# Optimization experiments

Hardware: AMD Instinct MI355X
Metric: run time of the kernel (lower is better)

Reference implementation:

```python
import jax, jax.numpy as jnp
import numpy as np

B, H, W, C = 32, 56, 56, 384
NH, WS, SS = 12, 7, 3
DH = C // NH
N = WS * WS
HID = 4 * C
SCALE = DH ** -0.5


def _make_attn_mask(h, w, ws, ss):
    img = np.zeros((h, w), dtype=np.float32)
    cnt = 0
    for hs in (slice(0, -ws), slice(-ws, -ss), slice(-ss, None)):
        for wsl in (slice(0, -ws), slice(-ws, -ss), slice(-ss, None)):
            img[hs, wsl] = cnt
            cnt += 1
    mw = img.reshape(h // ws, ws, w // ws, ws).transpose(0, 2, 1, 3).reshape(-1, ws * ws)
    diff = mw[:, None, :] - mw[:, :, None]  # (nW, n, n)
    return np.where(diff != 0, np.float32(-100.0), np.float32(0.0))


def _make_rel_pos_index(ws):
    coords = np.stack(np.meshgrid(np.arange(ws), np.arange(ws), indexing='ij')).reshape(2, -1)
    rel = (coords[:, :, None] - coords[:, None, :]).transpose(1, 2, 0)  # (n, n, 2)
    rel[..., 0] += ws - 1
    rel[..., 1] += ws - 1
    rel[..., 0] *= 2 * ws - 1
    return rel.sum(-1)  # (n, n)


ATTN_MASK = jnp.asarray(_make_attn_mask(H, W, WS, SS))          # (nW, n, n)
REL_IDX = jnp.asarray(_make_rel_pos_index(WS))                   # (n, n)


def layernorm(x, g, b, eps):
    mu = jnp.mean(x, axis=-1, keepdims=True)
    var = jnp.var(x, axis=-1, keepdims=True)
    return (x - mu) * jax.lax.rsqrt(var + eps) * g + b


def window_partition(x, ws):
    b, h, w, c = x.shape
    x = x.reshape(b, h // ws, ws, w // ws, ws, c)
    return x.transpose(0, 1, 3, 2, 4, 5).reshape(-1, ws, ws, c)


def window_reverse(windows, ws, h, w):
    b = windows.shape[0] // ((h // ws) * (w // ws))
    x = windows.reshape(b, h // ws, w // ws, ws, ws, -1)
    return x.transpose(0, 1, 3, 2, 4, 5).reshape(b, h, w, -1)


def setup_inputs() -> dict:
    key = jax.random.key(0)
    ks = jax.random.split(key, 8)
    d = {
        'x': jax.random.normal(ks[0], (B, H * W, C), dtype=jnp.float32),
        'ln1_g': jnp.ones((C,), jnp.float32), 'ln1_b': jnp.zeros((C,), jnp.float32),
        'qkv_w': jax.random.normal(ks[1], (C, 3 * C), jnp.float32) * 0.02,
        'qkv_b': jnp.zeros((3 * C,), jnp.float32),
        'proj_w': jax.random.normal(ks[2], (C, C), jnp.float32) * 0.02,
        'proj_b': jnp.zeros((C,), jnp.float32),
        'rpb_table': jax.random.normal(ks[3], ((2 * WS - 1) ** 2, NH), jnp.float32) * 0.02,
        'ln2_g': jnp.ones((C,), jnp.float32), 'ln2_b': jnp.zeros((C,), jnp.float32),
        'ffln_g': jnp.ones((C,), jnp.float32), 'ffln_b': jnp.zeros((C,), jnp.float32),
        'ff1_w': jax.random.normal(ks[4], (C, HID), jnp.float32) * 0.02,
        'ff1_b': jnp.zeros((HID,), jnp.float32),
        'ff2_w': jax.random.normal(ks[5], (HID, C), jnp.float32) * 0.02,
        'ff2_b': jnp.zeros((C,), jnp.float32),
    }
    return d


def reference(x, ln1_g, ln1_b, qkv_w, qkv_b, proj_w, proj_b, rpb_table,
              ln2_g, ln2_b, ffln_g, ffln_b, ff1_w, ff1_b, ff2_w, ff2_b):
    b = x.shape[0]
    shortcut = x
    xn = layernorm(x, ln1_g, ln1_b, 1e-5).reshape(b, H, W, C)
    shifted = jnp.roll(xn, shift=(-SS, -SS), axis=(1, 2))
    xw = window_partition(shifted, WS).reshape(-1, N, C)  # (b*nW, n, c)
    Bw = xw.shape[0]
    nW = Bw // b

    qkv = (xw @ qkv_w + qkv_b).reshape(Bw, N, 3, NH, DH).transpose(2, 0, 3, 1, 4)
    q, k, v = qkv[0], qkv[1], qkv[2]  # (Bw, nh, n, dh)
    dots = jnp.einsum('bhnd,bhmd->bhnm', q, k) * SCALE

    bias = rpb_table[REL_IDX.reshape(-1)].reshape(N, N, NH).transpose(2, 0, 1)  # (nh, n, n)
    attn = dots + bias[None]
    attn = attn.reshape(b, nW, NH, N, N) + ATTN_MASK[None, :, None, :, :]
    attn = jax.nn.softmax(attn.reshape(Bw, NH, N, N), axis=-1)

    out = jnp.einsum('bhnm,bhmd->bhnd', attn, v)
    out = out.transpose(0, 2, 1, 3).reshape(Bw, N, C)
    out = out @ proj_w + proj_b

    out = window_reverse(out.reshape(-1, WS, WS, C), WS, H, W)
    out = jnp.roll(out, shift=(SS, SS), axis=(1, 2)).reshape(b, H * W, C)

    x = shortcut + out
    y = layernorm(x, ln2_g, ln2_b, 1e-5)
    y = layernorm(y, ffln_g, ffln_b, 1e-6)
    y = jax.nn.gelu(y @ ff1_w + ff1_b, approximate=False) @ ff2_w + ff2_b
    return x + y
```

## Files before the change

### kernel.cpp

```cpp
#include <hip/hip_runtime.h>
#include <hip/hip_bf16.h>

typedef short bf16x8 __attribute__((ext_vector_type(8)));
typedef float f32x4  __attribute__((ext_vector_type(4)));

static constexpr float SCALE = 0.17677669529663687f;

__device__ __forceinline__ void gload_lds16(const void* g, void* l) {
  __builtin_amdgcn_global_load_lds(
      (const __attribute__((address_space(1))) unsigned int*)g,
      (__attribute__((address_space(3))) unsigned int*)l, 16, 0, 0);
}

__device__ __forceinline__ size_t win_to_nat(int t) {
  int win = t / 49; int n = t - win * 49;
  int bb = win >> 6; int wimg = win & 63;
  int hb = wimg >> 3, wb = wimg & 7;
  int nr = n / 7, nc = n - nr * 7;
  int hh = hb * 7 + nr + 3; if (hh >= 56) hh -= 56;
  int ww = wb * 7 + nc + 3; if (ww >= 56) ww -= 56;
  return (size_t)bb * 3136 + (size_t)hh * 56 + ww;
}

__global__ __launch_bounds__(256)
void k_transpose(const float* __restrict__ W, __hip_bfloat16* __restrict__ Wt,
                 int K, int N) {
  __shared__ float tile[32][33];
  int tx = threadIdx.x & 31, ty = threadIdx.x >> 5;
  int tc = blockIdx.x, tr = blockIdx.y;
#pragma unroll
  for (int r = 0; r < 32; r += 8)
    tile[r + ty][tx] = W[(size_t)(tr * 32 + r + ty) * N + tc * 32 + tx];
  __syncthreads();
#pragma unroll
  for (int r = 0; r < 32; r += 8)
    Wt[(size_t)(tc * 32 + r + ty) * K + tr * 32 + tx] =
        __float2bfloat16(tile[tx][r + ty]);
}

__global__ __launch_bounds__(256)
void k_ln1(const float* __restrict__ x, const float* __restrict__ gw,
           const float* __restrict__ bw, __hip_bfloat16* __restrict__ xw) {
  int lane = threadIdx.x & 63;
  int t = blockIdx.x * 4 + (threadIdx.x >> 6);
  size_t nt = win_to_nat(t);
  const float* xr = x + nt * 384;
  float4 a  = *(const float4*)(xr + lane * 4);
  float2 c2 = *(const float2*)(xr + 256 + lane * 2);
  float v[6] = {a.x, a.y, a.z, a.w, c2.x, c2.y};
  int c0 = lane * 4, c1 = 256 + lane * 2;
  int ch[6] = {c0, c0 + 1, c0 + 2, c0 + 3, c1, c1 + 1};
  float s = 0.f, q = 0.f;
#pragma unroll
  for (int i = 0; i < 6; i++) { s += v[i]; q += v[i] * v[i]; }
#pragma unroll
  for (int m = 1; m < 64; m <<= 1) { s += __shfl_xor(s, m); q += __shfl_xor(q, m); }
  float mean = s * (1.f / 384.f);
  float rstd = rsqrtf(q * (1.f / 384.f) - mean * mean + 1e-5f);
  __hip_bfloat16* o = xw + (size_t)t * 384;
#pragma unroll
  for (int i = 0; i < 6; i++)
    o[ch[i]] = __float2bfloat16((v[i] - mean) * rstd * gw[ch[i]] + bw[ch[i]]);
}

__global__ __launch_bounds__(256)
void k_ln2ff(const float* __restrict__ xres, const float* __restrict__ g2,
             const float* __restrict__ b2, const float* __restrict__ gf,
             const float* __restrict__ bf_, __hip_bfloat16* __restrict__ yln) {
  int lane = threadIdx.x & 63;
  int t = blockIdx.x * 4 + (threadIdx.x >> 6);
  const float* xr = xres + (size_t)t * 384;
  float4 a  = *(const float4*)(xr + lane * 4);
  float2 c2 = *(const float2*)(xr + 256 + lane * 2);
  float v[6] = {a.x, a.y, a.z, a.w, c2.x, c2.y};
  int c0 = lane * 4, c1 = 256 + lane * 2;
  int ch[6] = {c0, c0 + 1, c0 + 2, c0 + 3, c1, c1 + 1};
  float s = 0.f, q = 0.f;
#pragma unroll
  for (int i = 0; i < 6; i++) { s += v[i]; q += v[i] * v[i]; }
#pragma unroll
  for (int m = 1; m < 64; m <<= 1) { s += __shfl_xor(s, m); q += __shfl_xor(q, m); }
  float mean = s * (1.f / 384.f);
  float rstd = rsqrtf(q * (1.f / 384.f) - mean * mean + 1e-5f);
  float y1[6];
  s = 0.f; q = 0.f;
#pragma unroll
  for (int i = 0; i < 6; i++) {
    y1[i] = (v[i] - mean) * rstd * g2[ch[i]] + b2[ch[i]];
    s += y1[i]; q += y1[i] * y1[i];
  }
#pragma unroll
  for (int m = 1; m < 64; m <<= 1) { s += __shfl_xor(s, m); q += __shfl_xor(q, m); }
  float m2 = s * (1.f / 384.f);
  float r2 = rsqrtf(q * (1.f / 384.f) - m2 * m2 + 1e-6f);
  __hip_bfloat16* o = yln + (size_t)t * 384;
#pragma unroll
  for (int i = 0; i < 6; i++)
    o[ch[i]] = __float2bfloat16((y1[i] - m2) * r2 * gf[ch[i]] + bf_[ch[i]]);
}

enum { EPI_QKV = 0, EPI_PROJ = 1, EPI_FF1 = 2, EPI_FF2 = 3 };

template <int EPI>
__global__ __launch_bounds__(256)
void k_gemm(const __hip_bfloat16* __restrict__ A, const __hip_bfloat16* __restrict__ Wt,
            const float* __restrict__ bias, int K, int nCol, int cpx,
            const float* __restrict__ aux,
            float* __restrict__ out_f,
            __hip_bfloat16* __restrict__ out_b) {
  __shared__ __hip_bfloat16 As[2][8192];
  __shared__ __hip_bfloat16 Bs[2][8192];
  int tid = threadIdx.x;
  int lane = tid & 63, w = tid >> 6;
  int g = lane >> 4, r16 = lane & 15;
  int wr = w >> 1, wc = w & 1;

  int bid = blockIdx.x;
  int wg = (bid & 7) * cpx + (bid >> 3);
  int rB = wg / nCol;
  int rowBlk = rB * 128;
  int colBlk = (wg - rB * nCol) * 128;

  int srow = tid >> 3;
  int cch = (tid & 7) ^ (srow & 7);
  const __hip_bfloat16* PA = A + (size_t)(rowBlk + srow) * K + cch * 8;
  const __hip_bfloat16* PB = Wt + (size_t)(colBlk + srow) * K + cch * 8;

#define STG(NB, T)                                                      \
  {                                                                     \
    int k0s = (T) << 6;                                                 \
    _Pragma("unroll") for (int j = 0; j < 4; j++) {                     \
      gload_lds16(PA + (size_t)j * 32 * K + k0s, &As[NB][j * 2048 + w * 512]); \
      gload_lds16(PB + (size_t)j * 32 * K + k0s, &Bs[NB][j * 2048 + w * 512]); \
    }                                                                   \
  }

  int aBase = (wr * 64 + r16) * 64;
  int bBase = (wc * 64 + r16) * 64;
  int sw0 = (g ^ (r16 & 7)) * 8;
  int sw1 = ((4 + g) ^ (r16 & 7)) * 8;

  f32x4 acc[4][4] = {};
  const int nt = K >> 6;

  STG(0, 0)

  for (int t = 0; t < nt; ++t) {
    int cur = t & 1;
    if (t + 1 < nt) {
      STG(cur ^ 1, t + 1)
      asm volatile("s_waitcnt vmcnt(8)" ::: "memory");
    } else {
      asm volatile("s_waitcnt vmcnt(0)" ::: "memory");
    }
    __builtin_amdgcn_s_barrier();

    bf16x8 a0[4], a1[4], b0[4], b1[4];
#pragma unroll
    for (int mi = 0; mi < 4; mi++) {
      a0[mi] = *(const bf16x8*)(&As[cur][aBase + mi * 1024 + sw0]);
      a1[mi] = *(const bf16x8*)(&As[cur][aBase + mi * 1024 + sw1]);
    }
#pragma unroll
    for (int ni = 0; ni < 4; ni++) {
      b0[ni] = *(const bf16x8*)(&Bs[cur][bBase + ni * 1024 + sw0]);
      b1[ni] = *(const bf16x8*)(&Bs[cur][bBase + ni * 1024 + sw1]);
    }
    __builtin_amdgcn_s_setprio(1);
#pragma unroll
    for (int mi = 0; mi < 4; mi++)
#pragma unroll
      for (int ni = 0; ni < 4; ni++) {
        acc[mi][ni] = __builtin_amdgcn_mfma_f32_16x16x32_bf16(a0[mi], b0[ni], acc[mi][ni], 0, 0, 0);
        acc[mi][ni] = __builtin_amdgcn_mfma_f32_16x16x32_bf16(a1[mi], b1[ni], acc[mi][ni], 0, 0, 0);
      }
    __builtin_amdgcn_s_setprio(0);
    __builtin_amdgcn_s_barrier();
  }
#undef STG

#pragma unroll
  for (int mi = 0; mi < 4; mi++) {
#pragma unroll
    for (int rr = 0; rr < 4; rr++) {
      int row = rowBlk + wr * 64 + mi * 16 + g * 4 + rr;
      int winr = 0, nn = 0; size_t nt2 = 0;
      if constexpr (EPI == EPI_QKV) { winr = row / 49; nn = row - winr * 49; }
      if constexpr (EPI == EPI_PROJ) { nt2 = win_to_nat(row); }
#pragma unroll
      for (int ni = 0; ni < 4; ni++) {
        int col = colBlk + wc * 64 + ni * 16 + r16;
        float val = acc[mi][ni][rr] + bias[col];
        if constexpr (EPI == EPI_QKV) {
          int which = col / 384; int rem = col - which * 384;
          int hh = rem >> 5, dd = rem & 31;
          size_t off = (((size_t)winr * 12 + hh) * 49 + nn) * 32 + dd;
          out_b[(size_t)which * 38535168u + off] = __float2bfloat16(val);
        } else if constexpr (EPI == EPI_PROJ) {
          out_f[nt2 * 384 + col] = val + aux[nt2 * 384 + col];
        } else if constexpr (EPI == EPI_FF1) {
          float u = val * (val * val * 0.044715f + 1.0f) * 1.5957691216f;
          float e = __expf(u);
          float th = 1.f - 2.f / (e + 1.f);
          float ge = 0.5f * val * (1.f + th);
          out_b[(size_t)row * 1536 + col] = __float2bfloat16(ge);
        } else {
          out_f[(size_t)row * 384 + col] = val + aux[(size_t)row * 384 + col];
        }
      }
    }
  }
}

__global__ __launch_bounds__(256)
void k_attn(const __hip_bfloat16* __restrict__ q, const __hip_bfloat16* __restrict__ k,
            const __hip_bfloat16* __restrict__ v, const float* __restrict__ rpb,
            __hip_bfloat16* __restrict__ o) {
  __shared__ __hip_bfloat16 P[4][64][72];
  int tid = threadIdx.x;
  int lane = tid & 63, wave = tid >> 6;
  int g = lane >> 4, r16 = lane & 15;
  int gid = blockIdx.x * 4 + wave;
  int wi = gid / 12, h = gid - (gid / 12) * 12;
  int wimg = wi & 63;
  int hb = wimg >> 3, wb = wimg & 7;
  size_t base = ((size_t)wi * 12 + h) * (49 * 32);
  const __hip_bfloat16* qb = q + base;
  const __hip_bfloat16* kb = k + base;
  const __hip_bfloat16* vb = v + base;

  bf16x8 zf = {0, 0, 0, 0, 0, 0, 0, 0};
  bf16x8 qf[4], kf[4];
#pragma unroll
  for (int mi = 0; mi < 4; mi++) {
    int row = mi * 16 + r16;
    qf[mi] = (row < 49) ? *(const bf16x8*)(qb + row * 32 + g * 8) : zf;
    kf[mi] = (row < 49) ? *(const bf16x8*)(kb + row * 32 + g * 8) : zf;
  }
  f32x4 fz = {0.f, 0.f, 0.f, 0.f};
  f32x4 S[4][4];
#pragma unroll
  for (int mi = 0; mi < 4; mi++)
#pragma unroll
    for (int ni = 0; ni < 4; ni++)
      S[mi][ni] = __builtin_amdgcn_mfma_f32_16x16x32_bf16(qf[mi], kf[ni], fz, 0, 0, 0);

  int kiA[4], kjA[4], rkA[4], cvA[4];
#pragma unroll
  for (int ni = 0; ni < 4; ni++) {
    int col = ni * 16 + r16;
    cvA[ni] = (col < 49);
    int ki = col / 7, kj = col - (col / 7) * 7;
    kiA[ni] = ki; kjA[ni] = kj;
    int hg = hb * 7 + ki, wg = wb * 7 + kj;
    int rh = (hg < 49) ? 0 : ((hg < 53) ? 1 : 2);
    int rw = (wg < 49) ? 0 : ((wg < 53) ? 1 : 2);
    rkA[ni] = rh * 3 + rw;
  }

#pragma unroll
  for (int mi = 0; mi < 4; mi++) {
#pragma unroll
    for (int rr = 0; rr < 4; rr++) {
      int row = mi * 16 + g * 4 + rr;
      float sv[4];
      float mx = -1e30f;
      int qi = row / 7, qj = row - (row / 7) * 7;
      int hgq = hb * 7 + qi, wgq = wb * 7 + qj;
      int rhq = (hgq < 49) ? 0 : ((hgq < 53) ? 1 : 2);
      int rwq = (wgq < 49) ? 0 : ((wgq < 53) ? 1 : 2);
      int rq = rhq * 3 + rwq;
#pragma unroll
      for (int ni = 0; ni < 4; ni++) {
        float s = -1e30f;
        if (row < 49 && cvA[ni]) {
          int idx = (qi - kiA[ni] + 6) * 13 + (qj - kjA[ni] + 6);
          float maskv = (rq != rkA[ni]) ? -100.f : 0.f;
          s = S[mi][ni][rr] * SCALE + rpb[idx * 12 + h] + maskv;
        }
        sv[ni] = s;
        mx = fmaxf(mx, s);
      }
#pragma unroll
      for (int m = 1; m <= 8; m <<= 1) mx = fmaxf(mx, __shfl_xor(mx, m));
      float sum = 0.f;
#pragma unroll
      for (int ni = 0; ni < 4; ni++) {
        float p = __expf(sv[ni] - mx);
        sv[ni] = p; sum += p;
      }
#pragma unroll
      for (int m = 1; m <= 8; m <<= 1) sum += __shfl_xor(sum, m);
      float inv = 1.f / sum;
#pragma unroll
      for (int ni = 0; ni < 4; ni++)
        P[wave][row][ni * 16 + r16] = __float2bfloat16(sv[ni] * inv);
    }
  }

  f32x4 O[4][2] = {};
#pragma unroll
  for (int ks = 0; ks < 2; ks++) {
    bf16x8 pf[4];
#pragma unroll
    for (int mi = 0; mi < 4; mi++)
      pf[mi] = *(const bf16x8*)(&P[wave][mi * 16 + r16][ks * 32 + g * 8]);
#pragma unroll
    for (int ni = 0; ni < 2; ni++) {
      bf16x8 vf = zf;
#pragma unroll
      for (int j = 0; j < 8; j++) {
        int m = ks * 32 + g * 8 + j;
        if (m < 49) vf[j] = ((const short*)vb)[m * 32 + ni * 16 + r16];
      }
#pragma unroll
      for (int mi = 0; mi < 4; mi++)
        O[mi][ni] = __builtin_amdgcn_mfma_f32_16x16x32_bf16(pf[mi], vf, O[mi][ni], 0, 0, 0);
    }
  }

#pragma unroll
  for (int mi = 0; mi < 4; mi++)
#pragma unroll
    for (int rr = 0; rr < 4; rr++) {
      int row = mi * 16 + g * 4 + rr;
      if (row < 49) {
#pragma unroll
        for (int ni = 0; ni < 2; ni++) {
          int col = ni * 16 + r16;
          o[(((size_t)wi * 49 + row) * 12 + h) * 32 + col] = __float2bfloat16(O[mi][ni][rr]);
        }
      }
    }
}

extern "C" void kernel_launch(void* const* d_in, const int* in_sizes, int n_in,
                              void* d_out, int out_size, void* d_ws, size_t ws_size,
                              hipStream_t stream) {
  const float* x      = (const float*)d_in[0];
  const float* ln1_g  = (const float*)d_in[1];
  const float* ln1_b  = (const float*)d_in[2];
  const float* qkv_w  = (const float*)d_in[3];
  const float* qkv_b  = (const float*)d_in[4];
  const float* proj_w = (const float*)d_in[5];
  const float* proj_b = (const float*)d_in[6];
  const float* rpb    = (const float*)d_in[7];
  const float* ln2_g  = (const float*)d_in[8];
  const float* ln2_b  = (const float*)d_in[9];
  const float* ffg    = (const float*)d_in[10];
  const float* ffb    = (const float*)d_in[11];
  const float* ff1_w  = (const float*)d_in[12];
  const float* ff1_b  = (const float*)d_in[13];
  const float* ff2_w  = (const float*)d_in[14];
  const float* ff2_b  = (const float*)d_in[15];
  float* out = (float*)d_out;

  char* ws = (char*)d_ws;
  __hip_bfloat16* xw     = (__hip_bfloat16*)ws;
  __hip_bfloat16* qbuf   = (__hip_bfloat16*)(ws + 77070336u);
  __hip_bfloat16* kbuf   = qbuf + 38535168u;
  __hip_bfloat16* vbuf   = kbuf + 38535168u;
  __hip_bfloat16* attn_o = xw;
  __hip_bfloat16* hbuf   = (__hip_bfloat16*)ws;
  float*          x_res  = (float*)(ws + 308281344u);
  __hip_bfloat16* yln    = (__hip_bfloat16*)(ws + 462422016u);
  __hip_bfloat16* qkv_wt = (__hip_bfloat16*)(ws + 539492352u);
  __hip_bfloat16* proj_wt = qkv_wt + 442368u;
  __hip_bfloat16* ff1_wt  = proj_wt + 147456u;
  __hip_bfloat16* ff2_wt  = ff1_wt + 589824u;

  k_transpose<<<dim3(1152 / 32, 384 / 32), dim3(256), 0, stream>>>(qkv_w, qkv_wt, 384, 1152);
  k_transpose<<<dim3(384 / 32, 384 / 32), dim3(256), 0, stream>>>(proj_w, proj_wt, 384, 384);
  k_transpose<<<dim3(1536 / 32, 384 / 32), dim3(256), 0, stream>>>(ff1_w, ff1_wt, 384, 1536);
  k_transpose<<<dim3(384 / 32, 1536 / 32), dim3(256), 0, stream>>>(ff2_w, ff2_wt, 1536, 384);

  k_ln1<<<dim3(25088), dim3(256), 0, stream>>>(x, ln1_g, ln1_b, xw);

  k_gemm<EPI_QKV><<<dim3(7056), dim3(256), 0, stream>>>(xw, qkv_wt, qkv_b, 384, 9, 7056 / 8,
                                                        nullptr, nullptr, qbuf);
  k_attn<<<dim3(6144), dim3(256), 0, stream>>>(qbuf, kbuf, vbuf, rpb, attn_o);
  k_gemm<EPI_PROJ><<<dim3(2352), dim3(256), 0, stream>>>(attn_o, proj_wt, proj_b, 384, 3, 2352 / 8,
                                                         x, x_res, nullptr);
  k_ln2ff<<<dim3(25088), dim3(256), 0, stream>>>(x_res, ln2_g, ln2_b, ffg, ffb, yln);
  k_gemm<EPI_FF1><<<dim3(9408), dim3(256), 0, stream>>>(yln, ff1_wt, ff1_b, 384, 12, 9408 / 8,
                                                        nullptr, nullptr, hbuf);
  k_gemm<EPI_FF2><<<dim3(2352), dim3(256), 0, stream>>>(hbuf, ff2_wt, ff2_b, 1536, 3, 2352 / 8,
                                                        x_res, out, nullptr);
}
```

Measured before the change: 1.010 ms.

## Stage GEMM epilogue through LDS for vectorized coalesced global stores

The GEMM operand buffers are merged into one shared LDS array, and the MFMA operand order is swapped so each lane's accumulator holds four consecutive columns. After the main loop, each wave writes its biased (and, for FF1, GELU-applied) tile into its own swizzled LDS region. It then reads the tile back as 8-wide bf16 or 4-wide fp32 vectors for coalesced global stores and residual loads. This replaces scattered scalar stores in all four epilogues, at the cost of extra LDS traffic and register shuffling.

```diff
diff --git a/kernel.cpp b/kernel.cpp
--- a/kernel.cpp
+++ b/kernel.cpp
@@ -2,6 +2,7 @@
 #include <hip/hip_bf16.h>
 
 typedef short bf16x8 __attribute__((ext_vector_type(8)));
+typedef short short4v __attribute__((ext_vector_type(4)));
 typedef float f32x4  __attribute__((ext_vector_type(4)));
 
 static constexpr float SCALE = 0.17677669529663687f;
@@ -20,6 +21,13 @@
   int hh = hb * 7 + nr + 3; if (hh >= 56) hh -= 56;
   int ww = wb * 7 + nc + 3; if (ww >= 56) ww -= 56;
   return (size_t)bb * 3136 + (size_t)hh * 56 + ww;
+}
+
+__device__ __forceinline__ float gelu_tanh(float val) {
+  float u = val * (val * val * 0.044715f + 1.0f) * 1.5957691216f;
+  float e = __expf(u);
+  float th = 1.f - 2.f / (e + 1.f);
+  return 0.5f * val * (1.f + th);
 }
 
 __global__ __launch_bounds__(256)
@@ -108,8 +116,7 @@
             const float* __restrict__ aux,
             float* __restrict__ out_f,
             __hip_bfloat16* __restrict__ out_b) {
-  __shared__ __hip_bfloat16 As[2][8192];
-  __shared__ __hip_bfloat16 Bs[2][8192];
+  __shared__ __hip_bfloat16 LB[32768];
   int tid = threadIdx.x;
   int lane = tid & 63, w = tid >> 6;
   int g = lane >> 4, r16 = lane & 15;
@@ -126,13 +133,13 @@
   const __hip_bfloat16* PA = A + (size_t)(rowBlk + srow) * K + cch * 8;
   const __hip_bfloat16* PB = Wt + (size_t)(colBlk + srow) * K + cch * 8;
 
-#define STG(NB, T)                                                      \
-  {                                                                     \
-    int k0s = (T) << 6;                                                 \
-    _Pragma("unroll") for (int j = 0; j < 4; j++) {                     \
-      gload_lds16(PA + (size_t)j * 32 * K + k0s, &As[NB][j * 2048 + w * 512]); \
-      gload_lds16(PB + (size_t)j * 32 * K + k0s, &Bs[NB][j * 2048 + w * 512]); \
-    }                                                                   \
+#define STG(NB, T)                                                            \
+  {                                                                           \
+    int k0s = (T) << 6;                                                       \
+    _Pragma("unroll") for (int j = 0; j < 4; j++) {                           \
+      gload_lds16(PA + (size_t)j * 32 * K + k0s, &LB[(NB) * 8192 + j * 2048 + w * 512]); \
+      gload_lds16(PB + (size_t)j * 32 * K + k0s, &LB[16384 + (NB) * 8192 + j * 2048 + w * 512]); \
+    }                                                                         \
   }
 
   int aBase = (wr * 64 + r16) * 64;
@@ -158,55 +165,94 @@
     bf16x8 a0[4], a1[4], b0[4], b1[4];
 #pragma unroll
     for (int mi = 0; mi < 4; mi++) {
-      a0[mi] = *(const bf16x8*)(&As[cur][aBase + mi * 1024 + sw0]);
-      a1[mi] = *(const bf16x8*)(&As[cur][aBase + mi * 1024 + sw1]);
+      a0[mi] = *(const bf16x8*)(&LB[cur * 8192 + aBase + mi * 1024 + sw0]);
+      a1[mi] = *(const bf16x8*)(&LB[cur * 8192 + aBase + mi * 1024 + sw1]);
     }
 #pragma unroll
     for (int ni = 0; ni < 4; ni++) {
-      b0[ni] = *(const bf16x8*)(&Bs[cur][bBase + ni * 1024 + sw0]);
-      b1[ni] = *(const bf16x8*)(&Bs[cur][bBase + ni * 1024 + sw1]);
+      b0[ni] = *(const bf16x8*)(&LB[16384 + cur * 8192 + bBase + ni * 1024 + sw0]);
+      b1[ni] = *(const bf16x8*)(&LB[16384 + cur * 8192 + bBase + ni * 1024 + sw1]);
     }
     __builtin_amdgcn_s_setprio(1);
 #pragma unroll
     for (int mi = 0; mi < 4; mi++)
 #pragma unroll
       for (int ni = 0; ni < 4; ni++) {
-        acc[mi][ni] = __builtin_amdgcn_mfma_f32_16x16x32_bf16(a0[mi], b0[ni], acc[mi][ni], 0, 0, 0);
-        acc[mi][ni] = __builtin_amdgcn_mfma_f32_16x16x32_bf16(a1[mi], b1[ni], acc[mi][ni], 0, 0, 0);
+        acc[mi][ni] = __builtin_amdgcn_mfma_f32_16x16x32_bf16(b0[ni], a0[mi], acc[mi][ni], 0, 0, 0);
+        acc[mi][ni] = __builtin_amdgcn_mfma_f32_16x16x32_bf16(b1[ni], a1[mi], acc[mi][ni], 0, 0, 0);
       }
     __builtin_amdgcn_s_setprio(0);
     __builtin_amdgcn_s_barrier();
   }
 #undef STG
 
-#pragma unroll
-  for (int mi = 0; mi < 4; mi++) {
-#pragma unroll
-    for (int rr = 0; rr < 4; rr++) {
-      int row = rowBlk + wr * 64 + mi * 16 + g * 4 + rr;
-      int winr = 0, nn = 0; size_t nt2 = 0;
-      if constexpr (EPI == EPI_QKV) { winr = row / 49; nn = row - winr * 49; }
-      if constexpr (EPI == EPI_PROJ) { nt2 = win_to_nat(row); }
-#pragma unroll
-      for (int ni = 0; ni < 4; ni++) {
-        int col = colBlk + wc * 64 + ni * 16 + r16;
-        float val = acc[mi][ni][rr] + bias[col];
-        if constexpr (EPI == EPI_QKV) {
-          int which = col / 384; int rem = col - which * 384;
-          int hh = rem >> 5, dd = rem & 31;
-          size_t off = (((size_t)winr * 12 + hh) * 49 + nn) * 32 + dd;
-          out_b[(size_t)which * 38535168u + off] = __float2bfloat16(val);
-        } else if constexpr (EPI == EPI_PROJ) {
-          out_f[nt2 * 384 + col] = val + aux[nt2 * 384 + col];
-        } else if constexpr (EPI == EPI_FF1) {
-          float u = val * (val * val * 0.044715f + 1.0f) * 1.5957691216f;
-          float e = __expf(u);
-          float th = 1.f - 2.f / (e + 1.f);
-          float ge = 0.5f * val * (1.f + th);
-          out_b[(size_t)row * 1536 + col] = __float2bfloat16(ge);
-        } else {
-          out_f[(size_t)row * 384 + col] = val + aux[(size_t)row * 384 + col];
+  if constexpr (EPI == EPI_QKV || EPI == EPI_FF1) {
+    __hip_bfloat16* EP = &LB[w * 4096];
+#pragma unroll
+    for (int ni = 0; ni < 4; ni++) {
+      float4 b4 = *(const float4*)(bias + colBlk + wc * 64 + ni * 16 + g * 4);
+#pragma unroll
+      for (int mi = 0; mi < 4; mi++) {
+        float v0 = acc[mi][ni][0] + b4.x, v1 = acc[mi][ni][1] + b4.y,
+              v2 = acc[mi][ni][2] + b4.z, v3 = acc[mi][ni][3] + b4.w;
+        if constexpr (EPI == EPI_FF1) {
+          v0 = gelu_tanh(v0); v1 = gelu_tanh(v1);
+          v2 = gelu_tanh(v2); v3 = gelu_tanh(v3);
         }
+        short4v s4 = {(short)__bfloat16_as_ushort(__float2bfloat16(v0)),
+                      (short)__bfloat16_as_ushort(__float2bfloat16(v1)),
+                      (short)__bfloat16_as_ushort(__float2bfloat16(v2)),
+                      (short)__bfloat16_as_ushort(__float2bfloat16(v3))};
+        int row = mi * 16 + r16;
+        int ch8 = (ni * 2 + (g >> 1)) ^ (row & 7);
+        *(short4v*)(&EP[row * 64 + ch8 * 8 + (g & 1) * 4]) = s4;
+      }
+    }
+#pragma unroll
+    for (int j = 0; j < 8; j++) {
+      int r = j * 8 + (lane >> 3);
+      bf16x8 vv = *(const bf16x8*)(&EP[r * 64 + ((lane & 7) ^ (r & 7)) * 8]);
+      int grow = rowBlk + wr * 64 + r;
+      int col0 = colBlk + wc * 64 + (lane & 7) * 8;
+      if constexpr (EPI == EPI_QKV) {
+        int winr = grow / 49, nn = grow - winr * 49;
+        int which = col0 / 384; int rem = col0 - which * 384;
+        int hh = rem >> 5, dd = rem & 31;
+        size_t off = (((size_t)winr * 12 + hh) * 49 + nn) * 32 + dd;
+        *(bf16x8*)(out_b + (size_t)which * 38535168u + off) = vv;
+      } else {
+        *(bf16x8*)(out_b + (size_t)grow * 1536 + col0) = vv;
+      }
+    }
+  } else {
+    float* EPF = (float*)LB + w * 4096;
+#pragma unroll
+    for (int ni = 0; ni < 4; ni++) {
+      float4 b4 = *(const float4*)(bias + colBlk + wc * 64 + ni * 16 + g * 4);
+#pragma unroll
+      for (int mi = 0; mi < 4; mi++) {
+        f32x4 v = acc[mi][ni];
+        v[0] += b4.x; v[1] += b4.y; v[2] += b4.z; v[3] += b4.w;
+        int row = mi * 16 + r16;
+        int ch4 = (ni * 4 + g) ^ r16;
+        *(f32x4*)(&EPF[row * 64 + ch4 * 4]) = v;
+      }
+    }
+#pragma unroll
+    for (int j = 0; j < 16; j++) {
+      int r = j * 4 + g;
+      f32x4 vv = *(const f32x4*)(&EPF[r * 64 + ((r16 ^ (r & 15)) * 4)]);
+      int grow = rowBlk + wr * 64 + r;
+      int col0 = colBlk + wc * 64 + r16 * 4;
+      if constexpr (EPI == EPI_PROJ) {
+        size_t nt2 = win_to_nat(grow);
+        const float4 a4 = *(const float4*)(aux + nt2 * 384 + col0);
+        float4 o4 = {vv[0] + a4.x, vv[1] + a4.y, vv[2] + a4.z, vv[3] + a4.w};
+        *(float4*)(out_f + nt2 * 384 + col0) = o4;
+      } else {
+        const float4 a4 = *(const float4*)(aux + (size_t)grow * 384 + col0);
+        float4 o4 = {vv[0] + a4.x, vv[1] + a4.y, vv[2] + a4.z, vv[3] + a4.w};
+        *(float4*)(out_f + (size_t)grow * 384 + col0) = o4;
       }
     }
   }
```

Measured after the change: 905.9 us. 10.3% less time.
